# Kernel tuning notes

Measured on AMD Instinct MI355X. Metric: run time of the kernel, lower is better.

## Reference

```python
import jax, jax.numpy as jnp
import numpy as np

NT, NS, NH, NG = 365, 2048, 64, 128
PI = 3.1415  # constant used by the original code (not math.pi)


def setup_inputs() -> dict:
    key = jax.random.key(0)
    kP, kE, kTm, kdT, kxc, kW, kb = jax.random.split(key, 7)
    # Physically plausible forcings: positive precip/evap, T1 < T2 always
    P = jax.random.uniform(kP, (NT, NS)) * 20.0
    E = jax.random.uniform(kE, (NT, NS)) * 5.0
    Tm = jax.random.normal(kTm, (NT, NS)) * 10.0
    dT = jax.random.uniform(kdT, (NT, NS)) * 10.0 + 1.0
    T1 = Tm - dT / 2
    T2 = Tm + dT / 2
    x = jnp.stack([P, E, T1, T2], axis=-1)  # [nt, ns, 4]
    xc = jax.random.normal(kxc, (NS, NG))
    W = jax.random.normal(kW, (NH * 8 + 1, NG)) * 0.05  # fc weight
    b = jax.random.normal(kb, (NH * 8 + 1,)) * 0.05     # fc bias
    return {"x": x, "xc": xc, "W": W, "b": b}


def reference(x, xc, W, b):
    nh = (W.shape[0] - 1) // 8
    P, E, T1, T2 = x[..., 0], x[..., 1], x[..., 2], x[..., 3]  # each [nt, ns]
    Ta = (T1 + T2) / 2
    mask1 = T1 >= 0
    mask0 = T2 <= 0
    # nan-safe arccos argument: value is overwritten by the masks anyway
    arg = jnp.where(mask1 | mask0, 0.0, (T1 + T2) / (T2 - T1))
    rP = 1 - jnp.arccos(arg) / PI
    rP = jnp.where(mask1, 1.0, rP)
    rP = jnp.where(mask0, 0.0, rP)
    Ps = (1 - rP) * P  # snow
    Pl = rP * P        # liquid

    w = xc @ W.T + b  # [ns, nh*8+1]
    gm = jnp.exp(w[:, :nh]) + 1
    ge = jax.nn.sigmoid(w[:, nh:2 * nh]) * 2
    k0 = jax.nn.sigmoid(w[:, 3 * nh:4 * nh])
    k1 = jax.nn.sigmoid(w[:, 4 * nh:5 * nh])
    k2 = jax.nn.sigmoid(w[:, 5 * nh:6 * nh])
    gl = jnp.exp(w[:, 6 * nh:7 * nh])
    ga = jax.nn.softmax(w[:, 4 * nh:5 * nh], axis=1)  # dropout in eval = id
    qb = jax.nn.relu(w[:, -1]) / nh  # [ns]
    kb = jax.nn.sigmoid(w[:, 7 * nh:8 * nh]) / 10
    vi = jax.nn.sigmoid(w[:, 8 * nh:8 * nh + 1])  # (ns, 1) — faithful to source slice

    ns = P.shape[1]
    z = jnp.zeros((ns, nh), dtype=x.dtype)

    def step(carry, inp):
        S0, H0, H1, H2 = carry
        ps, pl, e, ta = inp  # each [ns]
        S = S0 + ps[:, None]
        Sm = jnp.minimum(S0, jax.nn.relu(ta[:, None] * gm))
        G1 = jax.nn.relu(H1 + Sm + pl[:, None] * vi - e[:, None] * ge)
        G0 = jax.nn.relu(H0 + G1 - gl + pl[:, None] * (1 - vi))
        Q0 = G0 * k0
        Q1a = jnp.minimum(G1, gl) * k1
        Q1 = Q1a * (1 - kb)
        G2 = H2 + Q1a * kb
        Q2 = G2 * k2
        Y = jnp.sum((Q0 + Q1 + Q2 + qb[:, None]) * ga, axis=1)
        return (S - Sm, G0 - Q0, jnp.minimum(G1 - Q1a, gl), G2 - Q2), Y

    _, Yout = jax.lax.scan(step, (z, z, z, z), (Ps, Pl, E, Ta))
    return Yout  # [nt, ns]
```

## Files before the change

kernel.cpp:

```cpp
#include <hip/hip_runtime.h>
#include <math.h>

#define NT 365
#define NS 2048
#define NH 64
#define NG 128
#define NW 513
#define WSTR 520

__device__ __forceinline__ float sigmoidf_(float x) {
    return 1.0f / (1.0f + __expf(-x));
}

__global__ __launch_bounds__(256) void forcing_kernel(const float* __restrict__ x,
                                                      float* __restrict__ f, int n) {
    int i = blockIdx.x * blockDim.x + threadIdx.x;
    if (i >= n) return;
    float4 v = ((const float4*)x)[i];
    float P = v.x, E = v.y, T1 = v.z, T2 = v.w;
    float Ta = 0.5f * (T1 + T2);
    float rP;
    if (T2 <= 0.0f)       rP = 0.0f;
    else if (T1 >= 0.0f)  rP = 1.0f;
    else                  rP = 1.0f - acosf((T1 + T2) / (T2 - T1)) * (1.0f / 3.1415f);
    float Ps = (1.0f - rP) * P;
    float Pl = rP * P;
    ((float4*)f)[i] = make_float4(Ps, Pl, E, fmaxf(Ta, 0.0f));
}

__global__ __launch_bounds__(256) void gemm_kernel(const float* __restrict__ xc,
                                                   const float* __restrict__ Wm,
                                                   const float* __restrict__ bv,
                                                   float* __restrict__ w) {
    __shared__ float xcs[64][132];
    __shared__ float Wsh[64][132];
    const int sTile = blockIdx.x * 64;
    const int by = blockIdx.y;
    const int jt = (by >= 2) ? by + 1 : by;
    const int jTile = jt * 64;
    const int t = threadIdx.x;

    for (int i = 0; i < 8; i++) {
        int f4  = t + i * 256;
        int row = f4 >> 5;
        int c4  = (f4 & 31) * 4;
        float4 v = ((const float4*)(xc + (size_t)(sTile + row) * NG))[f4 & 31];
        xcs[row][c4] = v.x; xcs[row][c4 + 1] = v.y; xcs[row][c4 + 2] = v.z; xcs[row][c4 + 3] = v.w;
        int jr = jTile + row;
        float4 wv = make_float4(0.f, 0.f, 0.f, 0.f);
        if (jr < NW) wv = ((const float4*)(Wm + (size_t)jr * NG))[f4 & 31];
        Wsh[row][c4] = wv.x; Wsh[row][c4 + 1] = wv.y; Wsh[row][c4 + 2] = wv.z; Wsh[row][c4 + 3] = wv.w;
    }
    __syncthreads();

    const int tx = t & 15, ty = t >> 4;
    float acc[4][4] = {};
#pragma unroll 4
    for (int k = 0; k < 128; k++) {
        float a0 = xcs[ty][k], a1 = xcs[ty + 16][k], a2 = xcs[ty + 32][k], a3 = xcs[ty + 48][k];
        float b0 = Wsh[tx][k], b1 = Wsh[tx + 16][k], b2 = Wsh[tx + 32][k], b3 = Wsh[tx + 48][k];
        acc[0][0] += a0 * b0; acc[0][1] += a0 * b1; acc[0][2] += a0 * b2; acc[0][3] += a0 * b3;
        acc[1][0] += a1 * b0; acc[1][1] += a1 * b1; acc[1][2] += a1 * b2; acc[1][3] += a1 * b3;
        acc[2][0] += a2 * b0; acc[2][1] += a2 * b1; acc[2][2] += a2 * b2; acc[2][3] += a2 * b3;
        acc[3][0] += a3 * b0; acc[3][1] += a3 * b1; acc[3][2] += a3 * b2; acc[3][3] += a3 * b3;
    }
#pragma unroll
    for (int i = 0; i < 4; i++) {
        int s = sTile + ty + 16 * i;
#pragma unroll
        for (int j = 0; j < 4; j++) {
            int jj = jTile + tx + 16 * j;
            if (jj < NW) w[(size_t)s * WSTR + jj] = acc[i][j] + bv[jj];
        }
    }
}

template <bool PRE>
__global__ __launch_bounds__(256) void scan_kernel(const float* __restrict__ fx,
                                                   const float* __restrict__ w,
                                                   float* __restrict__ Y) {
    __shared__ float ybuf[4][64][33];
    const int wave = threadIdx.x >> 6;
    const int lane = threadIdx.x & 63;
    const int s = blockIdx.x * 4 + wave;
    const float* wr = w + (size_t)s * WSTR;

    float gm = __expf(wr[lane]) + 1.0f;
    float ge = 2.0f * sigmoidf_(wr[64 + lane]);
    float k0 = sigmoidf_(wr[192 + lane]);
    float w4 = wr[256 + lane];
    float k1 = sigmoidf_(w4);
    float k2 = sigmoidf_(wr[320 + lane]);
    float gl = __expf(wr[384 + lane]);
    float kb = sigmoidf_(wr[448 + lane]) * 0.1f;
    float wl = wr[512];
    float qb = fmaxf(wl, 0.0f) * (1.0f / (float)NH);
    float vi = sigmoidf_(wl);

    float m = w4;
#pragma unroll
    for (int off = 32; off; off >>= 1) m = fmaxf(m, __shfl_xor(m, off));
    float ex = __expf(w4 - m);
    float sum = ex;
#pragma unroll
    for (int off = 32; off; off >>= 1) sum += __shfl_xor(sum, off);
    float ga = ex / sum;

    float c0  = k0 * ga;
    float c1  = k1 * (1.0f - kb) * ga;
    float c2  = k2 * ga;
    float k0c = 1.0f - k0;
    float k2c = 1.0f - k2;
    float geN = -ge;
    float glN = -gl;
    float viC = 1.0f - vi;

    float S0 = 0.f, H0 = 0.f, H1 = 0.f, H2 = 0.f;

    const int su = __builtin_amdgcn_readfirstlane(s);
    const float4* fp = (const float4*)fx + su;

    float* wp = &ybuf[wave][lane][0];
    const float* rp = &ybuf[wave][(lane >> 5) << 5][lane & 31];

    float4 vbuf[8];
#pragma unroll
    for (int b = 0; b < 8; b++) vbuf[b] = fp[b * NS];

    for (int sb = 0; sb < 12; sb++) {
        const int t0 = sb * 32;
        for (int ib = 0; ib < 4; ib++) {
#pragma unroll
            for (int b = 0; b < 8; b++) {
                const int tl = ib * 8 + b;
                float4 v = vbuf[b];
                int tn = t0 + (ib + 1) * 8 + b;
                tn = tn < NT ? tn : NT - 1;
                vbuf[b] = fp[(size_t)tn * NS];

                float Ps, Pl, E, TaR;
                if (PRE) {
                    Ps = v.x; Pl = v.y; E = v.z; TaR = v.w;
                } else {
                    float P = v.x; E = v.y;
                    float T1 = v.z, T2 = v.w;
                    float Ta = 0.5f * (T1 + T2);
                    float rP;
                    if (T2 <= 0.0f)      rP = 0.0f;
                    else if (T1 >= 0.0f) rP = 1.0f;
                    else                 rP = 1.0f - acosf((T1 + T2) / (T2 - T1)) * (1.0f / 3.1415f);
                    Ps = (1.0f - rP) * P;
                    Pl = rP * P;
                    TaR = fmaxf(Ta, 0.0f);
                }
                float S   = S0 + Ps;
                float Sm  = fminf(S0, gm * TaR);
                S0 = S - Sm;
                float G1  = fmaxf(H1 + Sm + fmaf(E, geN, Pl * vi), 0.0f);
                float G0  = fmaxf(H0 + G1 + fmaf(Pl, viC, glN), 0.0f);
                float m1  = fminf(G1, gl);
                float Q1a = m1 * k1;
                float G2  = fmaf(Q1a, kb, H2);
                wp[tl] = fmaf(G0, c0, fmaf(m1, c1, G2 * c2));
                H0 = G0 * k0c;
                H1 = fminf(G1 - Q1a, gl);
                H2 = G2 * k2c;
            }
        }
        float a0 = 0.f, a1 = 0.f, a2 = 0.f, a3 = 0.f;
#pragma unroll
        for (int j = 0; j < 32; j += 4) {
            a0 += rp[(size_t)j * 33];
            a1 += rp[(size_t)(j + 1) * 33];
            a2 += rp[(size_t)(j + 2) * 33];
            a3 += rp[(size_t)(j + 3) * 33];
        }
        float part = (a0 + a1) + (a2 + a3);
        float full = part + __shfl_xor(part, 32);
        int t = t0 + lane;
        if (lane < 32 && t < NT) Y[(size_t)t * NS + s] = full + qb;
    }
}

extern "C" void kernel_launch(void* const* d_in, const int* in_sizes, int n_in,
                              void* d_out, int out_size, void* d_ws, size_t ws_size,
                              hipStream_t stream) {
    const float* x  = (const float*)d_in[0];
    const float* xc = (const float*)d_in[1];
    const float* Wm = (const float*)d_in[2];
    const float* bv = (const float*)d_in[3];
    float* out = (float*)d_out;

    float* wbuf = (float*)d_ws;
    size_t wbytes = (size_t)NS * WSTR * sizeof(float);
    float* fbuf = (float*)((char*)d_ws + wbytes);
    size_t need = wbytes + (size_t)NT * NS * 4 * sizeof(float);

    gemm_kernel<<<dim3(32, 8), 256, 0, stream>>>(xc, Wm, bv, wbuf);

    if (ws_size >= need) {
        forcing_kernel<<<(NT * NS + 255) / 256, 256, 0, stream>>>(x, fbuf, NT * NS);
        scan_kernel<true><<<NS / 4, 256, 0, stream>>>(fbuf, wbuf, out);
    } else {
        scan_kernel<false><<<NS / 4, 256, 0, stream>>>(x, wbuf, out);
    }
}
```

Measured before the change: 121.8 us.

## Fuse gemm and forcing kernels; process two sites per wave in scan

Merges the parameter GEMM and the forcing precompute into one launch so one kernel launch and a dependency gap go away. The scan kernel now handles two sites per wavefront and interleaves their independent recurrences. This adds instruction-level parallelism to the latency-bound serial time loop and lets all 64 lanes take part in the final reduction. The cost is half as many blocks (256), which lowers occupancy and wave count on a large GPU, plus higher register and LDS use.

```diff
diff --git a/kernel.cpp b/kernel.cpp
--- a/kernel.cpp
+++ b/kernel.cpp
@@ -12,36 +12,38 @@
     return 1.0f / (1.0f + __expf(-x));
 }
 
-__global__ __launch_bounds__(256) void forcing_kernel(const float* __restrict__ x,
-                                                      float* __restrict__ f, int n) {
-    int i = blockIdx.x * blockDim.x + threadIdx.x;
-    if (i >= n) return;
-    float4 v = ((const float4*)x)[i];
-    float P = v.x, E = v.y, T1 = v.z, T2 = v.w;
-    float Ta = 0.5f * (T1 + T2);
-    float rP;
-    if (T2 <= 0.0f)       rP = 0.0f;
-    else if (T1 >= 0.0f)  rP = 1.0f;
-    else                  rP = 1.0f - acosf((T1 + T2) / (T2 - T1)) * (1.0f / 3.1415f);
-    float Ps = (1.0f - rP) * P;
-    float Pl = rP * P;
-    ((float4*)f)[i] = make_float4(Ps, Pl, E, fmaxf(Ta, 0.0f));
-}
-
-__global__ __launch_bounds__(256) void gemm_kernel(const float* __restrict__ xc,
+__global__ __launch_bounds__(256) void prep_kernel(const float* __restrict__ xc,
                                                    const float* __restrict__ Wm,
                                                    const float* __restrict__ bv,
-                                                   float* __restrict__ w) {
+                                                   float* __restrict__ w,
+                                                   const float* __restrict__ x,
+                                                   float* __restrict__ f) {
     __shared__ float xcs[64][132];
     __shared__ float Wsh[64][132];
-    const int sTile = blockIdx.x * 64;
-    const int by = blockIdx.y;
+    const int tid = threadIdx.x;
+
+    if (blockIdx.x >= 256) {
+        int i = (blockIdx.x - 256) * 256 + tid;
+        float4 v = ((const float4*)x)[i];
+        float P = v.x, E = v.y, T1 = v.z, T2 = v.w;
+        float Ta = 0.5f * (T1 + T2);
+        float rP;
+        if (T2 <= 0.0f)       rP = 0.0f;
+        else if (T1 >= 0.0f)  rP = 1.0f;
+        else                  rP = 1.0f - acosf((T1 + T2) / (T2 - T1)) * (1.0f / 3.1415f);
+        float Ps = (1.0f - rP) * P;
+        float Pl = rP * P;
+        ((float4*)f)[i] = make_float4(Ps, Pl, E, fmaxf(Ta, 0.0f));
+        return;
+    }
+
+    const int sTile = (blockIdx.x >> 3) * 64;
+    const int by = blockIdx.x & 7;
     const int jt = (by >= 2) ? by + 1 : by;
     const int jTile = jt * 64;
-    const int t = threadIdx.x;
 
     for (int i = 0; i < 8; i++) {
-        int f4  = t + i * 256;
+        int f4  = tid + i * 256;
         int row = f4 >> 5;
         int c4  = (f4 & 31) * 4;
         float4 v = ((const float4*)(xc + (size_t)(sTile + row) * NG))[f4 & 31];
@@ -53,7 +55,7 @@
     }
     __syncthreads();
 
-    const int tx = t & 15, ty = t >> 4;
+    const int tx = tid & 15, ty = tid >> 4;
     float acc[4][4] = {};
 #pragma unroll 4
     for (int k = 0; k < 128; k++) {
@@ -79,53 +81,61 @@
 __global__ __launch_bounds__(256) void scan_kernel(const float* __restrict__ fx,
                                                    const float* __restrict__ w,
                                                    float* __restrict__ Y) {
-    __shared__ float ybuf[4][64][33];
+    __shared__ float ybuf[4][2][64][33];
     const int wave = threadIdx.x >> 6;
     const int lane = threadIdx.x & 63;
-    const int s = blockIdx.x * 4 + wave;
-    const float* wr = w + (size_t)s * WSTR;
-
-    float gm = __expf(wr[lane]) + 1.0f;
-    float ge = 2.0f * sigmoidf_(wr[64 + lane]);
-    float k0 = sigmoidf_(wr[192 + lane]);
-    float w4 = wr[256 + lane];
-    float k1 = sigmoidf_(w4);
-    float k2 = sigmoidf_(wr[320 + lane]);
-    float gl = __expf(wr[384 + lane]);
-    float kb = sigmoidf_(wr[448 + lane]) * 0.1f;
-    float wl = wr[512];
-    float qb = fmaxf(wl, 0.0f) * (1.0f / (float)NH);
-    float vi = sigmoidf_(wl);
-
-    float m = w4;
-#pragma unroll
-    for (int off = 32; off; off >>= 1) m = fmaxf(m, __shfl_xor(m, off));
-    float ex = __expf(w4 - m);
-    float sum = ex;
-#pragma unroll
-    for (int off = 32; off; off >>= 1) sum += __shfl_xor(sum, off);
-    float ga = ex / sum;
-
-    float c0  = k0 * ga;
-    float c1  = k1 * (1.0f - kb) * ga;
-    float c2  = k2 * ga;
-    float k0c = 1.0f - k0;
-    float k2c = 1.0f - k2;
-    float geN = -ge;
-    float glN = -gl;
-    float viC = 1.0f - vi;
-
-    float S0 = 0.f, H0 = 0.f, H1 = 0.f, H2 = 0.f;
-
-    const int su = __builtin_amdgcn_readfirstlane(s);
+    const int sA = blockIdx.x * 8 + wave * 2;
+    const float* wrA = w + (size_t)sA * WSTR;
+    const float* wrB = wrA + WSTR;
+
+    float gmA = __expf(wrA[lane]) + 1.0f,          gmB = __expf(wrB[lane]) + 1.0f;
+    float geNA = -2.0f * sigmoidf_(wrA[64 + lane]), geNB = -2.0f * sigmoidf_(wrB[64 + lane]);
+    float k0A = sigmoidf_(wrA[192 + lane]),        k0B = sigmoidf_(wrB[192 + lane]);
+    float w4A = wrA[256 + lane],                   w4B = wrB[256 + lane];
+    float k1A = sigmoidf_(w4A),                    k1B = sigmoidf_(w4B);
+    float k2A = sigmoidf_(wrA[320 + lane]),        k2B = sigmoidf_(wrB[320 + lane]);
+    float glA = __expf(wrA[384 + lane]),           glB = __expf(wrB[384 + lane]);
+    float kbA = sigmoidf_(wrA[448 + lane]) * 0.1f, kbB = sigmoidf_(wrB[448 + lane]) * 0.1f;
+    float wlA = wrA[512],                          wlB = wrB[512];
+    float qbA = fmaxf(wlA, 0.0f) * (1.0f / NH),    qbB = fmaxf(wlB, 0.0f) * (1.0f / NH);
+    float viA = sigmoidf_(wlA),                    viB = sigmoidf_(wlB);
+
+    float mA = w4A, mB = w4B;
+#pragma unroll
+    for (int off = 32; off; off >>= 1) {
+        mA = fmaxf(mA, __shfl_xor(mA, off));
+        mB = fmaxf(mB, __shfl_xor(mB, off));
+    }
+    float exA = __expf(w4A - mA), exB = __expf(w4B - mB);
+    float smA = exA, smB = exB;
+#pragma unroll
+    for (int off = 32; off; off >>= 1) {
+        smA += __shfl_xor(smA, off);
+        smB += __shfl_xor(smB, off);
+    }
+    float gaA = exA / smA, gaB = exB / smB;
+
+    float c0A = k0A * gaA,                  c0B = k0B * gaB;
+    float c1A = k1A * (1.0f - kbA) * gaA,   c1B = k1B * (1.0f - kbB) * gaB;
+    float c2A = k2A * gaA,                  c2B = k2B * gaB;
+    float k0cA = 1.0f - k0A,                k0cB = 1.0f - k0B;
+    float k2cA = 1.0f - k2A,                k2cB = 1.0f - k2B;
+    float glNA = -glA,                      glNB = -glB;
+    float viCA = 1.0f - viA,                viCB = 1.0f - viB;
+
+    float S0A = 0.f, H0A = 0.f, H1A = 0.f, H2A = 0.f;
+    float S0B = 0.f, H0B = 0.f, H1B = 0.f, H2B = 0.f;
+
+    const int su = __builtin_amdgcn_readfirstlane(sA);
     const float4* fp = (const float4*)fx + su;
 
-    float* wp = &ybuf[wave][lane][0];
-    const float* rp = &ybuf[wave][(lane >> 5) << 5][lane & 31];
-
-    float4 vbuf[8];
-#pragma unroll
-    for (int b = 0; b < 8; b++) vbuf[b] = fp[b * NS];
+    float* wp = &ybuf[wave][0][lane][0];
+    const float* rp = &ybuf[wave][lane >> 5][0][lane & 31];
+    const float qbS = (lane < 32) ? qbA : qbB;
+
+    float4 vbA[8], vbB[8];
+#pragma unroll
+    for (int b = 0; b < 8; b++) { vbA[b] = fp[b * NS]; vbB[b] = fp[b * NS + 1]; }
 
     for (int sb = 0; sb < 12; sb++) {
         const int t0 = sb * 32;
@@ -133,52 +143,75 @@
 #pragma unroll
             for (int b = 0; b < 8; b++) {
                 const int tl = ib * 8 + b;
-                float4 v = vbuf[b];
+                float4 vA = vbA[b], vB = vbB[b];
                 int tn = t0 + (ib + 1) * 8 + b;
                 tn = tn < NT ? tn : NT - 1;
-                vbuf[b] = fp[(size_t)tn * NS];
-
-                float Ps, Pl, E, TaR;
+                vbA[b] = fp[(size_t)tn * NS];
+                vbB[b] = fp[(size_t)tn * NS + 1];
+
+                float PsA, PlA, EA, TaRA, PsB, PlB, EB, TaRB;
                 if (PRE) {
-                    Ps = v.x; Pl = v.y; E = v.z; TaR = v.w;
+                    PsA = vA.x; PlA = vA.y; EA = vA.z; TaRA = vA.w;
+                    PsB = vB.x; PlB = vB.y; EB = vB.z; TaRB = vB.w;
                 } else {
-                    float P = v.x; E = v.y;
-                    float T1 = v.z, T2 = v.w;
-                    float Ta = 0.5f * (T1 + T2);
-                    float rP;
-                    if (T2 <= 0.0f)      rP = 0.0f;
-                    else if (T1 >= 0.0f) rP = 1.0f;
-                    else                 rP = 1.0f - acosf((T1 + T2) / (T2 - T1)) * (1.0f / 3.1415f);
-                    Ps = (1.0f - rP) * P;
-                    Pl = rP * P;
-                    TaR = fmaxf(Ta, 0.0f);
+                    {
+                        float P = vA.x; EA = vA.y;
+                        float T1 = vA.z, T2 = vA.w;
+                        float Ta = 0.5f * (T1 + T2);
+                        float rP;
+                        if (T2 <= 0.0f)      rP = 0.0f;
+                        else if (T1 >= 0.0f) rP = 1.0f;
+                        else                 rP = 1.0f - acosf((T1 + T2) / (T2 - T1)) * (1.0f / 3.1415f);
+                        PsA = (1.0f - rP) * P; PlA = rP * P; TaRA = fmaxf(Ta, 0.0f);
+                    }
+                    {
+                        float P = vB.x; EB = vB.y;
+                        float T1 = vB.z, T2 = vB.w;
+                        float Ta = 0.5f * (T1 + T2);
+                        float rP;
+                        if (T2 <= 0.0f)      rP = 0.0f;
+                        else if (T1 >= 0.0f) rP = 1.0f;
+                        else                 rP = 1.0f - acosf((T1 + T2) / (T2 - T1)) * (1.0f / 3.1415f);
+                        PsB = (1.0f - rP) * P; PlB = rP * P; TaRB = fmaxf(Ta, 0.0f);
+                    }
                 }
-                float S   = S0 + Ps;
-                float Sm  = fminf(S0, gm * TaR);
-                S0 = S - Sm;
-                float G1  = fmaxf(H1 + Sm + fmaf(E, geN, Pl * vi), 0.0f);
-                float G0  = fmaxf(H0 + G1 + fmaf(Pl, viC, glN), 0.0f);
-                float m1  = fminf(G1, gl);
-                float Q1a = m1 * k1;
-                float G2  = fmaf(Q1a, kb, H2);
-                wp[tl] = fmaf(G0, c0, fmaf(m1, c1, G2 * c2));
-                H0 = G0 * k0c;
-                H1 = fminf(G1 - Q1a, gl);
-                H2 = G2 * k2c;
+                float SA   = S0A + PsA;
+                float SmA  = fminf(S0A, gmA * TaRA);
+                S0A = SA - SmA;
+                float G1A  = fmaxf(H1A + SmA + fmaf(EA, geNA, PlA * viA), 0.0f);
+                float G0A  = fmaxf(H0A + G1A + fmaf(PlA, viCA, glNA), 0.0f);
+                float m1A  = fminf(G1A, glA);
+                float Q1aA = m1A * k1A;
+                float G2A  = fmaf(Q1aA, kbA, H2A);
+                wp[tl] = fmaf(G0A, c0A, fmaf(m1A, c1A, G2A * c2A));
+                H0A = G0A * k0cA;
+                H1A = fminf(G1A - Q1aA, glA);
+                H2A = G2A * k2cA;
+                float SB   = S0B + PsB;
+                float SmB  = fminf(S0B, gmB * TaRB);
+                S0B = SB - SmB;
+                float G1B  = fmaxf(H1B + SmB + fmaf(EB, geNB, PlB * viB), 0.0f);
+                float G0B  = fmaxf(H0B + G1B + fmaf(PlB, viCB, glNB), 0.0f);
+                float m1B  = fminf(G1B, glB);
+                float Q1aB = m1B * k1B;
+                float G2B  = fmaf(Q1aB, kbB, H2B);
+                wp[64 * 33 + tl] = fmaf(G0B, c0B, fmaf(m1B, c1B, G2B * c2B));
+                H0B = G0B * k0cB;
+                H1B = fminf(G1B - Q1aB, glB);
+                H2B = G2B * k2cB;
             }
         }
         float a0 = 0.f, a1 = 0.f, a2 = 0.f, a3 = 0.f;
 #pragma unroll
-        for (int j = 0; j < 32; j += 4) {
+        for (int j = 0; j < 64; j += 4) {
             a0 += rp[(size_t)j * 33];
             a1 += rp[(size_t)(j + 1) * 33];
             a2 += rp[(size_t)(j + 2) * 33];
             a3 += rp[(size_t)(j + 3) * 33];
         }
-        float part = (a0 + a1) + (a2 + a3);
-        float full = part + __shfl_xor(part, 32);
-        int t = t0 + lane;
-        if (lane < 32 && t < NT) Y[(size_t)t * NS + s] = full + qb;
+        float full = (a0 + a1) + (a2 + a3);
+        int t = t0 + (lane & 31);
+        if (t < NT) Y[(size_t)t * NS + sA + (lane >> 5)] = full + qbS;
     }
 }
 
@@ -196,12 +229,11 @@
     float* fbuf = (float*)((char*)d_ws + wbytes);
     size_t need = wbytes + (size_t)NT * NS * 4 * sizeof(float);
 
-    gemm_kernel<<<dim3(32, 8), 256, 0, stream>>>(xc, Wm, bv, wbuf);
-
     if (ws_size >= need) {
-        forcing_kernel<<<(NT * NS + 255) / 256, 256, 0, stream>>>(x, fbuf, NT * NS);
-        scan_kernel<true><<<NS / 4, 256, 0, stream>>>(fbuf, wbuf, out);
+        prep_kernel<<<256 + (NT * NS) / 256, 256, 0, stream>>>(xc, Wm, bv, wbuf, x, fbuf);
+        scan_kernel<true><<<NS / 8, 256, 0, stream>>>(fbuf, wbuf, out);
     } else {
-        scan_kernel<false><<<NS / 4, 256, 0, stream>>>(x, wbuf, out);
-    }
-}
+        prep_kernel<<<256, 256, 0, stream>>>(xc, Wm, bv, wbuf, x, fbuf);
+        scan_kernel<false><<<NS / 8, 256, 0, stream>>>(x, wbuf, out);
+    }
+}
```

After: 154.2 us. 1.27x slower.

## Merge GEMM and forcing kernels into one launch and unroll scan loop fully

Applied to the files above, without the earlier changes.

The separate GEMM and forcing-preprocess kernels become a single prep kernel: blocks beyond the first 256 handle forcing, the rest do the GEMM. This removes one launch and lets both run concurrently. The scan loop is now fully unrolled over 32 steps, and the time-index clamp is hoisted out of every block except the last. The base pointer is also kept in a vector register through an asm barrier instead of readfirstlane. In exchange the unrolled code is much larger and may raise register pressure.

```diff
diff --git a/kernel.cpp b/kernel.cpp
--- a/kernel.cpp
+++ b/kernel.cpp
@@ -12,36 +12,38 @@
     return 1.0f / (1.0f + __expf(-x));
 }
 
-__global__ __launch_bounds__(256) void forcing_kernel(const float* __restrict__ x,
-                                                      float* __restrict__ f, int n) {
-    int i = blockIdx.x * blockDim.x + threadIdx.x;
-    if (i >= n) return;
-    float4 v = ((const float4*)x)[i];
-    float P = v.x, E = v.y, T1 = v.z, T2 = v.w;
-    float Ta = 0.5f * (T1 + T2);
-    float rP;
-    if (T2 <= 0.0f)       rP = 0.0f;
-    else if (T1 >= 0.0f)  rP = 1.0f;
-    else                  rP = 1.0f - acosf((T1 + T2) / (T2 - T1)) * (1.0f / 3.1415f);
-    float Ps = (1.0f - rP) * P;
-    float Pl = rP * P;
-    ((float4*)f)[i] = make_float4(Ps, Pl, E, fmaxf(Ta, 0.0f));
-}
-
-__global__ __launch_bounds__(256) void gemm_kernel(const float* __restrict__ xc,
+__global__ __launch_bounds__(256) void prep_kernel(const float* __restrict__ xc,
                                                    const float* __restrict__ Wm,
                                                    const float* __restrict__ bv,
-                                                   float* __restrict__ w) {
+                                                   float* __restrict__ w,
+                                                   const float* __restrict__ x,
+                                                   float* __restrict__ f) {
     __shared__ float xcs[64][132];
     __shared__ float Wsh[64][132];
-    const int sTile = blockIdx.x * 64;
-    const int by = blockIdx.y;
+    const int tid = threadIdx.x;
+
+    if (blockIdx.x >= 256) {
+        int i = (blockIdx.x - 256) * 256 + tid;
+        float4 v = ((const float4*)x)[i];
+        float P = v.x, E = v.y, T1 = v.z, T2 = v.w;
+        float Ta = 0.5f * (T1 + T2);
+        float rP;
+        if (T2 <= 0.0f)       rP = 0.0f;
+        else if (T1 >= 0.0f)  rP = 1.0f;
+        else                  rP = 1.0f - acosf((T1 + T2) / (T2 - T1)) * (1.0f / 3.1415f);
+        float Ps = (1.0f - rP) * P;
+        float Pl = rP * P;
+        ((float4*)f)[i] = make_float4(Ps, Pl, E, fmaxf(Ta, 0.0f));
+        return;
+    }
+
+    const int sTile = (blockIdx.x >> 3) * 64;
+    const int by = blockIdx.x & 7;
     const int jt = (by >= 2) ? by + 1 : by;
     const int jTile = jt * 64;
-    const int t = threadIdx.x;
 
     for (int i = 0; i < 8; i++) {
-        int f4  = t + i * 256;
+        int f4  = tid + i * 256;
         int row = f4 >> 5;
         int c4  = (f4 & 31) * 4;
         float4 v = ((const float4*)(xc + (size_t)(sTile + row) * NG))[f4 & 31];
@@ -53,7 +55,7 @@
     }
     __syncthreads();
 
-    const int tx = t & 15, ty = t >> 4;
+    const int tx = tid & 15, ty = tid >> 4;
     float acc[4][4] = {};
 #pragma unroll 4
     for (int k = 0; k < 128; k++) {
@@ -86,7 +88,7 @@
     const float* wr = w + (size_t)s * WSTR;
 
     float gm = __expf(wr[lane]) + 1.0f;
-    float ge = 2.0f * sigmoidf_(wr[64 + lane]);
+    float geN = -2.0f * sigmoidf_(wr[64 + lane]);
     float k0 = sigmoidf_(wr[192 + lane]);
     float w4 = wr[256 + lane];
     float k1 = sigmoidf_(w4);
@@ -111,14 +113,14 @@
     float c2  = k2 * ga;
     float k0c = 1.0f - k0;
     float k2c = 1.0f - k2;
-    float geN = -ge;
     float glN = -gl;
     float viC = 1.0f - vi;
 
     float S0 = 0.f, H0 = 0.f, H1 = 0.f, H2 = 0.f;
 
-    const int su = __builtin_amdgcn_readfirstlane(s);
-    const float4* fp = (const float4*)fx + su;
+    int sv = s;
+    asm volatile("" : "+v"(sv));
+    const float4* fp = (const float4*)fx + sv;
 
     float* wp = &ybuf[wave][lane][0];
     const float* rp = &ybuf[wave][(lane >> 5) << 5][lane & 31];
@@ -127,59 +129,74 @@
 #pragma unroll
     for (int b = 0; b < 8; b++) vbuf[b] = fp[b * NS];
 
-    for (int sb = 0; sb < 12; sb++) {
+#define STEP_BODY(vv, tl)                                                      \
+    {                                                                          \
+        float Ps, Pl, E, TaR;                                                  \
+        if (PRE) { Ps = vv.x; Pl = vv.y; E = vv.z; TaR = vv.w; }               \
+        else {                                                                 \
+            float P = vv.x; E = vv.y;                                          \
+            float T1 = vv.z, T2 = vv.w;                                        \
+            float Ta = 0.5f * (T1 + T2);                                       \
+            float rP;                                                          \
+            if (T2 <= 0.0f)      rP = 0.0f;                                    \
+            else if (T1 >= 0.0f) rP = 1.0f;                                    \
+            else rP = 1.0f - acosf((T1 + T2) / (T2 - T1)) * (1.0f / 3.1415f);  \
+            Ps = (1.0f - rP) * P; Pl = rP * P; TaR = fmaxf(Ta, 0.0f);          \
+        }                                                                      \
+        float S   = S0 + Ps;                                                   \
+        float Sm  = fminf(S0, gm * TaR);                                       \
+        S0 = S - Sm;                                                           \
+        float G1  = fmaxf(H1 + Sm + fmaf(E, geN, Pl * vi), 0.0f);              \
+        float G0  = fmaxf(H0 + G1 + fmaf(Pl, viC, glN), 0.0f);                 \
+        float m1  = fminf(G1, gl);                                             \
+        float Q1a = m1 * k1;                                                   \
+        float G2  = fmaf(Q1a, kb, H2);                                         \
+        wp[tl] = fmaf(G0, c0, fmaf(m1, c1, G2 * c2));                          \
+        H0 = G0 * k0c;                                                         \
+        H1 = fminf(G1 - Q1a, gl);                                              \
+        H2 = G2 * k2c;                                                         \
+    }
+
+#define TRRED(t0)                                                              \
+    {                                                                          \
+        float a0 = 0.f, a1 = 0.f, a2 = 0.f, a3 = 0.f;                          \
+        _Pragma("unroll")                                                      \
+        for (int j = 0; j < 32; j += 4) {                                      \
+            a0 += rp[(size_t)j * 33];                                          \
+            a1 += rp[(size_t)(j + 1) * 33];                                    \
+            a2 += rp[(size_t)(j + 2) * 33];                                    \
+            a3 += rp[(size_t)(j + 3) * 33];                                    \
+        }                                                                      \
+        float part = (a0 + a1) + (a2 + a3);                                    \
+        float full = part + __shfl_xor(part, 32);                              \
+        int t = (t0) + (lane & 31);                                            \
+        if (lane < 32 && t < NT) Y[(size_t)t * NS + s] = full + qb;            \
+    }
+
+    for (int sb = 0; sb < 11; ++sb) {
         const int t0 = sb * 32;
-        for (int ib = 0; ib < 4; ib++) {
-#pragma unroll
-            for (int b = 0; b < 8; b++) {
-                const int tl = ib * 8 + b;
-                float4 v = vbuf[b];
-                int tn = t0 + (ib + 1) * 8 + b;
-                tn = tn < NT ? tn : NT - 1;
-                vbuf[b] = fp[(size_t)tn * NS];
-
-                float Ps, Pl, E, TaR;
-                if (PRE) {
-                    Ps = v.x; Pl = v.y; E = v.z; TaR = v.w;
-                } else {
-                    float P = v.x; E = v.y;
-                    float T1 = v.z, T2 = v.w;
-                    float Ta = 0.5f * (T1 + T2);
-                    float rP;
-                    if (T2 <= 0.0f)      rP = 0.0f;
-                    else if (T1 >= 0.0f) rP = 1.0f;
-                    else                 rP = 1.0f - acosf((T1 + T2) / (T2 - T1)) * (1.0f / 3.1415f);
-                    Ps = (1.0f - rP) * P;
-                    Pl = rP * P;
-                    TaR = fmaxf(Ta, 0.0f);
-                }
-                float S   = S0 + Ps;
-                float Sm  = fminf(S0, gm * TaR);
-                S0 = S - Sm;
-                float G1  = fmaxf(H1 + Sm + fmaf(E, geN, Pl * vi), 0.0f);
-                float G0  = fmaxf(H0 + G1 + fmaf(Pl, viC, glN), 0.0f);
-                float m1  = fminf(G1, gl);
-                float Q1a = m1 * k1;
-                float G2  = fmaf(Q1a, kb, H2);
-                wp[tl] = fmaf(G0, c0, fmaf(m1, c1, G2 * c2));
-                H0 = G0 * k0c;
-                H1 = fminf(G1 - Q1a, gl);
-                H2 = G2 * k2c;
-            }
+        const float4* fpt = fp + (size_t)t0 * NS;
+#pragma unroll
+        for (int tl = 0; tl < 32; ++tl) {
+            float4 v = vbuf[tl & 7];
+            vbuf[tl & 7] = fpt[(size_t)(tl + 8) * NS];
+            STEP_BODY(v, tl);
         }
-        float a0 = 0.f, a1 = 0.f, a2 = 0.f, a3 = 0.f;
-#pragma unroll
-        for (int j = 0; j < 32; j += 4) {
-            a0 += rp[(size_t)j * 33];
-            a1 += rp[(size_t)(j + 1) * 33];
-            a2 += rp[(size_t)(j + 2) * 33];
-            a3 += rp[(size_t)(j + 3) * 33];
+        TRRED(t0);
+    }
+    {
+        const int t0 = 352;
+#pragma unroll
+        for (int tl = 0; tl < 32; ++tl) {
+            float4 v = vbuf[tl & 7];
+            int tn = t0 + tl + 8; tn = tn < NT ? tn : NT - 1;
+            vbuf[tl & 7] = fp[(size_t)tn * NS];
+            STEP_BODY(v, tl);
         }
-        float part = (a0 + a1) + (a2 + a3);
-        float full = part + __shfl_xor(part, 32);
-        int t = t0 + lane;
-        if (lane < 32 && t < NT) Y[(size_t)t * NS + s] = full + qb;
-    }
+        TRRED(t0);
+    }
+#undef STEP_BODY
+#undef TRRED
 }
 
 extern "C" void kernel_launch(void* const* d_in, const int* in_sizes, int n_in,
@@ -196,12 +213,11 @@
     float* fbuf = (float*)((char*)d_ws + wbytes);
     size_t need = wbytes + (size_t)NT * NS * 4 * sizeof(float);
 
-    gemm_kernel<<<dim3(32, 8), 256, 0, stream>>>(xc, Wm, bv, wbuf);
-
     if (ws_size >= need) {
-        forcing_kernel<<<(NT * NS + 255) / 256, 256, 0, stream>>>(x, fbuf, NT * NS);
+        prep_kernel<<<256 + (NT * NS) / 256, 256, 0, stream>>>(xc, Wm, bv, wbuf, x, fbuf);
         scan_kernel<true><<<NS / 4, 256, 0, stream>>>(fbuf, wbuf, out);
     } else {
+        prep_kernel<<<256, 256, 0, stream>>>(xc, Wm, bv, wbuf, x, fbuf);
         scan_kernel<false><<<NS / 4, 256, 0, stream>>>(x, wbuf, out);
     }
 }
```

After: 110.1 us. -9.6%, faster.

## Fuse forcing prep into GEMM launch and pack two sites per wave

Applied to the files above, without the earlier changes.

The forcing precompute is merged into the GEMM kernel as extra blocks, which removes one launch. Forcings are written in a per-site-pair, time-contiguous layout so the scan reads them with contiguous loads. The scan now has each wave process two sites together using 2-wide float vectors, aiming at packed FP32 math, and prefetches 16 steps ahead. In exchange, the scan launches half as many waves, which reduces parallelism, and it uses more registers under launch_bounds(256,1).

```diff
diff --git a/kernel.cpp b/kernel.cpp
--- a/kernel.cpp
+++ b/kernel.cpp
@@ -7,41 +7,71 @@
 #define NG 128
 #define NW 513
 #define WSTR 520
+#define FTR 368
+
+typedef float v2f __attribute__((ext_vector_type(2)));
 
 __device__ __forceinline__ float sigmoidf_(float x) {
     return 1.0f / (1.0f + __expf(-x));
 }
-
-__global__ __launch_bounds__(256) void forcing_kernel(const float* __restrict__ x,
-                                                      float* __restrict__ f, int n) {
-    int i = blockIdx.x * blockDim.x + threadIdx.x;
-    if (i >= n) return;
-    float4 v = ((const float4*)x)[i];
-    float P = v.x, E = v.y, T1 = v.z, T2 = v.w;
-    float Ta = 0.5f * (T1 + T2);
-    float rP;
-    if (T2 <= 0.0f)       rP = 0.0f;
-    else if (T1 >= 0.0f)  rP = 1.0f;
-    else                  rP = 1.0f - acosf((T1 + T2) / (T2 - T1)) * (1.0f / 3.1415f);
-    float Ps = (1.0f - rP) * P;
-    float Pl = rP * P;
-    ((float4*)f)[i] = make_float4(Ps, Pl, E, fmaxf(Ta, 0.0f));
-}
-
-__global__ __launch_bounds__(256) void gemm_kernel(const float* __restrict__ xc,
+__device__ __forceinline__ v2f vmin2(v2f a, v2f b) {
+    v2f r; r.x = fminf(a.x, b.x); r.y = fminf(a.y, b.y); return r;
+}
+__device__ __forceinline__ v2f vmax0(v2f a) {
+    v2f r; r.x = fmaxf(a.x, 0.0f); r.y = fmaxf(a.y, 0.0f); return r;
+}
+
+__global__ __launch_bounds__(256) void prep_kernel(const float* __restrict__ xc,
                                                    const float* __restrict__ Wm,
                                                    const float* __restrict__ bv,
-                                                   float* __restrict__ w) {
+                                                   float* __restrict__ w,
+                                                   const float* __restrict__ x,
+                                                   float* __restrict__ f) {
     __shared__ float xcs[64][132];
     __shared__ float Wsh[64][132];
-    const int sTile = blockIdx.x * 64;
-    const int by = blockIdx.y;
+    const int tid = threadIdx.x;
+
+    if (blockIdx.x >= 256) {
+        const int b = blockIdx.x - 256;
+        const int p = b * 16 + (tid >> 4);
+        const int phase = tid & 15;
+        const float4* xp = (const float4*)x;
+        float4* fpo = (float4*)(f + (size_t)p * (FTR * 8));
+        for (int tt = phase; tt < NT; tt += 16) {
+            float4 vA = xp[(size_t)tt * NS + 2 * p];
+            float4 vB = xp[(size_t)tt * NS + 2 * p + 1];
+            float PsA, PlA, TaRA, PsB, PlB, TaRB;
+            {
+                float P = vA.x, T1 = vA.z, T2 = vA.w;
+                float Ta = 0.5f * (T1 + T2);
+                float rP;
+                if (T2 <= 0.0f)       rP = 0.0f;
+                else if (T1 >= 0.0f)  rP = 1.0f;
+                else                  rP = 1.0f - acosf((T1 + T2) / (T2 - T1)) * (1.0f / 3.1415f);
+                PsA = (1.0f - rP) * P; PlA = rP * P; TaRA = fmaxf(Ta, 0.0f);
+            }
+            {
+                float P = vB.x, T1 = vB.z, T2 = vB.w;
+                float Ta = 0.5f * (T1 + T2);
+                float rP;
+                if (T2 <= 0.0f)       rP = 0.0f;
+                else if (T1 >= 0.0f)  rP = 1.0f;
+                else                  rP = 1.0f - acosf((T1 + T2) / (T2 - T1)) * (1.0f / 3.1415f);
+                PsB = (1.0f - rP) * P; PlB = rP * P; TaRB = fmaxf(Ta, 0.0f);
+            }
+            fpo[tt * 2]     = make_float4(PsA, PsB, PlA, PlB);
+            fpo[tt * 2 + 1] = make_float4(vA.y, vB.y, TaRA, TaRB);
+        }
+        return;
+    }
+
+    const int sTile = (blockIdx.x >> 3) * 64;
+    const int by = blockIdx.x & 7;
     const int jt = (by >= 2) ? by + 1 : by;
     const int jTile = jt * 64;
-    const int t = threadIdx.x;
 
     for (int i = 0; i < 8; i++) {
-        int f4  = t + i * 256;
+        int f4  = tid + i * 256;
         int row = f4 >> 5;
         int c4  = (f4 & 31) * 4;
         float4 v = ((const float4*)(xc + (size_t)(sTile + row) * NG))[f4 & 31];
@@ -53,7 +83,7 @@
     }
     __syncthreads();
 
-    const int tx = t & 15, ty = t >> 4;
+    const int tx = tid & 15, ty = tid >> 4;
     float acc[4][4] = {};
 #pragma unroll 4
     for (int k = 0; k < 128; k++) {
@@ -75,10 +105,134 @@
     }
 }
 
-template <bool PRE>
-__global__ __launch_bounds__(256) void scan_kernel(const float* __restrict__ fx,
-                                                   const float* __restrict__ w,
-                                                   float* __restrict__ Y) {
+__global__ __launch_bounds__(256, 1) void scan_pk_kernel(const float* __restrict__ fx,
+                                                         const float* __restrict__ w,
+                                                         float* __restrict__ Y) {
+    __shared__ float ybuf[4][64][66];
+    const int wave = threadIdx.x >> 6;
+    const int lane = threadIdx.x & 63;
+    const int pair = blockIdx.x * 4 + wave;
+    const int sA = pair * 2;
+    const float* wrA = w + (size_t)sA * WSTR;
+    const float* wrB = wrA + WSTR;
+
+    v2f gm  = { __expf(wrA[lane]) + 1.0f,        __expf(wrB[lane]) + 1.0f };
+    v2f geN = { -2.0f * sigmoidf_(wrA[64 + lane]), -2.0f * sigmoidf_(wrB[64 + lane]) };
+    v2f k0  = { sigmoidf_(wrA[192 + lane]),      sigmoidf_(wrB[192 + lane]) };
+    v2f w4  = { wrA[256 + lane],                 wrB[256 + lane] };
+    v2f k1  = { sigmoidf_(w4.x),                 sigmoidf_(w4.y) };
+    v2f k2  = { sigmoidf_(wrA[320 + lane]),      sigmoidf_(wrB[320 + lane]) };
+    v2f gl  = { __expf(wrA[384 + lane]),         __expf(wrB[384 + lane]) };
+    v2f kb  = { sigmoidf_(wrA[448 + lane]) * 0.1f, sigmoidf_(wrB[448 + lane]) * 0.1f };
+    float wlA = wrA[512], wlB = wrB[512];
+    float qbA = fmaxf(wlA, 0.0f) * (1.0f / NH), qbB = fmaxf(wlB, 0.0f) * (1.0f / NH);
+    v2f vi  = { sigmoidf_(wlA),                  sigmoidf_(wlB) };
+
+    float mA = w4.x, mB = w4.y;
+#pragma unroll
+    for (int off = 32; off; off >>= 1) {
+        mA = fmaxf(mA, __shfl_xor(mA, off));
+        mB = fmaxf(mB, __shfl_xor(mB, off));
+    }
+    float exA = __expf(w4.x - mA), exB = __expf(w4.y - mB);
+    float smA = exA, smB = exB;
+#pragma unroll
+    for (int off = 32; off; off >>= 1) {
+        smA += __shfl_xor(smA, off);
+        smB += __shfl_xor(smB, off);
+    }
+    v2f ga = { exA / smA, exB / smB };
+
+    v2f one = { 1.0f, 1.0f };
+    v2f c0   = k0 * ga;
+    v2f c1   = k1 * (one - kb) * ga;
+    v2f c2   = k2 * ga;
+    v2f k0c  = one - k0;
+    v2f k2c  = one - k2;
+    v2f glN  = -gl;
+    v2f viC  = one - vi;
+    v2f k1kb = k1 * kb;
+    v2f k1N  = -k1;
+
+    v2f S0 = {0.f, 0.f}, H0 = {0.f, 0.f}, H1 = {0.f, 0.f}, H2 = {0.f, 0.f};
+
+    const char* fB = (const char*)fx;
+    unsigned voff = (unsigned)pair * (FTR * 32u);
+    asm volatile("" : "+v"(voff));
+
+    float4 va[16], vb[16];
+#pragma unroll
+    for (int b = 0; b < 16; b++) {
+        va[b] = *(const float4*)(fB + voff + b * 32);
+        vb[b] = *(const float4*)(fB + voff + b * 32 + 16);
+    }
+
+    float* wp = &ybuf[wave][lane][0];
+    const float* rp = &ybuf[wave][(lane >> 5) << 5][(lane & 31) * 2];
+
+#define STEP_PK(v1, v2, tl)                                                    \
+    {                                                                          \
+        v2f Ps = {v1.x, v1.y}, Pl = {v1.z, v1.w};                              \
+        v2f E  = {v2.x, v2.y}, Ta = {v2.z, v2.w};                              \
+        v2f S  = S0 + Ps;                                                      \
+        v2f Sm = vmin2(S0, gm * Ta);                                           \
+        S0 = S - Sm;                                                           \
+        v2f G1 = vmax0(H1 + Sm + (E * geN + Pl * vi));                         \
+        v2f G0 = vmax0(H0 + G1 + (Pl * viC + glN));                            \
+        v2f m1 = vmin2(G1, gl);                                                \
+        v2f G2 = m1 * k1kb + H2;                                               \
+        *(v2f*)&wp[2 * (tl)] = G0 * c0 + (m1 * c1 + G2 * c2);                  \
+        H0 = G0 * k0c;                                                         \
+        H1 = vmin2(m1 * k1N + G1, gl);                                         \
+        H2 = G2 * k2c;                                                         \
+    }
+
+#define TRRED_PK(t0)                                                           \
+    {                                                                          \
+        v2f a0 = {0.f,0.f}, a1 = {0.f,0.f}, a2 = {0.f,0.f}, a3 = {0.f,0.f};    \
+        _Pragma("unroll")                                                      \
+        for (int j = 0; j < 32; j += 4) {                                      \
+            a0 += *(const v2f*)&rp[(size_t)j * 66];                            \
+            a1 += *(const v2f*)&rp[(size_t)(j + 1) * 66];                      \
+            a2 += *(const v2f*)&rp[(size_t)(j + 2) * 66];                      \
+            a3 += *(const v2f*)&rp[(size_t)(j + 3) * 66];                      \
+        }                                                                      \
+        v2f part = (a0 + a1) + (a2 + a3);                                      \
+        float fx_ = part.x + __shfl_xor(part.x, 32);                           \
+        float fy_ = part.y + __shfl_xor(part.y, 32);                           \
+        int t = (t0) + (lane & 31);                                            \
+        if (lane < 32 && t < NT) {                                             \
+            Y[(size_t)t * NS + sA]     = fx_ + qbA;                            \
+            Y[(size_t)t * NS + sA + 1] = fy_ + qbB;                            \
+        }                                                                      \
+    }
+
+    for (int sb = 0; sb < 11; ++sb) {
+        const char* fs = fB + sb * (32 * 32);
+#pragma unroll
+        for (int tl = 0; tl < 32; ++tl) {
+            float4 v1 = va[tl & 15], v2 = vb[tl & 15];
+            va[tl & 15] = *(const float4*)(fs + voff + (tl + 16) * 32);
+            vb[tl & 15] = *(const float4*)(fs + voff + (tl + 16) * 32 + 16);
+            STEP_PK(v1, v2, tl);
+        }
+        TRRED_PK(sb * 32);
+    }
+    {
+#pragma unroll
+        for (int tl = 0; tl < 32; ++tl) {
+            float4 v1 = va[tl & 15], v2 = vb[tl & 15];
+            STEP_PK(v1, v2, tl);
+        }
+        TRRED_PK(352);
+    }
+#undef STEP_PK
+#undef TRRED_PK
+}
+
+__global__ __launch_bounds__(256) void scan_kernel_raw(const float* __restrict__ fx,
+                                                       const float* __restrict__ w,
+                                                       float* __restrict__ Y) {
     __shared__ float ybuf[4][64][33];
     const int wave = threadIdx.x >> 6;
     const int lane = threadIdx.x & 63;
@@ -86,7 +240,7 @@
     const float* wr = w + (size_t)s * WSTR;
 
     float gm = __expf(wr[lane]) + 1.0f;
-    float ge = 2.0f * sigmoidf_(wr[64 + lane]);
+    float geN = -2.0f * sigmoidf_(wr[64 + lane]);
     float k0 = sigmoidf_(wr[192 + lane]);
     float w4 = wr[256 + lane];
     float k1 = sigmoidf_(w4);
@@ -106,66 +260,41 @@
     for (int off = 32; off; off >>= 1) sum += __shfl_xor(sum, off);
     float ga = ex / sum;
 
-    float c0  = k0 * ga;
-    float c1  = k1 * (1.0f - kb) * ga;
-    float c2  = k2 * ga;
-    float k0c = 1.0f - k0;
-    float k2c = 1.0f - k2;
-    float geN = -ge;
-    float glN = -gl;
-    float viC = 1.0f - vi;
-
+    float c0 = k0 * ga, c1 = k1 * (1.0f - kb) * ga, c2 = k2 * ga;
+    float k0c = 1.0f - k0, k2c = 1.0f - k2, glN = -gl, viC = 1.0f - vi;
+    float k1kb = k1 * kb, k1N = -k1;
     float S0 = 0.f, H0 = 0.f, H1 = 0.f, H2 = 0.f;
 
-    const int su = __builtin_amdgcn_readfirstlane(s);
-    const float4* fp = (const float4*)fx + su;
+    unsigned voff = (unsigned)s * 16u;
+    asm volatile("" : "+v"(voff));
+    const char* fB = (const char*)fx;
 
     float* wp = &ybuf[wave][lane][0];
     const float* rp = &ybuf[wave][(lane >> 5) << 5][lane & 31];
 
-    float4 vbuf[8];
-#pragma unroll
-    for (int b = 0; b < 8; b++) vbuf[b] = fp[b * NS];
-
-    for (int sb = 0; sb < 12; sb++) {
+    for (int sb = 0; sb < 12; ++sb) {
         const int t0 = sb * 32;
-        for (int ib = 0; ib < 4; ib++) {
-#pragma unroll
-            for (int b = 0; b < 8; b++) {
-                const int tl = ib * 8 + b;
-                float4 v = vbuf[b];
-                int tn = t0 + (ib + 1) * 8 + b;
-                tn = tn < NT ? tn : NT - 1;
-                vbuf[b] = fp[(size_t)tn * NS];
-
-                float Ps, Pl, E, TaR;
-                if (PRE) {
-                    Ps = v.x; Pl = v.y; E = v.z; TaR = v.w;
-                } else {
-                    float P = v.x; E = v.y;
-                    float T1 = v.z, T2 = v.w;
-                    float Ta = 0.5f * (T1 + T2);
-                    float rP;
-                    if (T2 <= 0.0f)      rP = 0.0f;
-                    else if (T1 >= 0.0f) rP = 1.0f;
-                    else                 rP = 1.0f - acosf((T1 + T2) / (T2 - T1)) * (1.0f / 3.1415f);
-                    Ps = (1.0f - rP) * P;
-                    Pl = rP * P;
-                    TaR = fmaxf(Ta, 0.0f);
-                }
-                float S   = S0 + Ps;
-                float Sm  = fminf(S0, gm * TaR);
-                S0 = S - Sm;
-                float G1  = fmaxf(H1 + Sm + fmaf(E, geN, Pl * vi), 0.0f);
-                float G0  = fmaxf(H0 + G1 + fmaf(Pl, viC, glN), 0.0f);
-                float m1  = fminf(G1, gl);
-                float Q1a = m1 * k1;
-                float G2  = fmaf(Q1a, kb, H2);
-                wp[tl] = fmaf(G0, c0, fmaf(m1, c1, G2 * c2));
-                H0 = G0 * k0c;
-                H1 = fminf(G1 - Q1a, gl);
-                H2 = G2 * k2c;
-            }
+        for (int tl = 0; tl < 32; ++tl) {
+            int t = t0 + tl; t = t < NT ? t : NT - 1;
+            float4 v = *(const float4*)(fB + (size_t)t * (NS * 16) + voff);
+            float P = v.x, E = v.y, T1 = v.z, T2 = v.w;
+            float Ta = 0.5f * (T1 + T2);
+            float rP;
+            if (T2 <= 0.0f)      rP = 0.0f;
+            else if (T1 >= 0.0f) rP = 1.0f;
+            else                 rP = 1.0f - acosf((T1 + T2) / (T2 - T1)) * (1.0f / 3.1415f);
+            float Ps = (1.0f - rP) * P, Pl = rP * P, TaR = fmaxf(Ta, 0.0f);
+            float S   = S0 + Ps;
+            float Sm  = fminf(S0, gm * TaR);
+            S0 = S - Sm;
+            float G1  = fmaxf(H1 + Sm + fmaf(E, geN, Pl * vi), 0.0f);
+            float G0  = fmaxf(H0 + G1 + fmaf(Pl, viC, glN), 0.0f);
+            float m1  = fminf(G1, gl);
+            float G2  = fmaf(m1, k1kb, H2);
+            wp[tl] = fmaf(G0, c0, fmaf(m1, c1, G2 * c2));
+            H0 = G0 * k0c;
+            H1 = fminf(fmaf(m1, k1N, G1), gl);
+            H2 = G2 * k2c;
         }
         float a0 = 0.f, a1 = 0.f, a2 = 0.f, a3 = 0.f;
 #pragma unroll
@@ -177,7 +306,7 @@
         }
         float part = (a0 + a1) + (a2 + a3);
         float full = part + __shfl_xor(part, 32);
-        int t = t0 + lane;
+        int t = t0 + (lane & 31);
         if (lane < 32 && t < NT) Y[(size_t)t * NS + s] = full + qb;
     }
 }
@@ -194,14 +323,13 @@
     float* wbuf = (float*)d_ws;
     size_t wbytes = (size_t)NS * WSTR * sizeof(float);
     float* fbuf = (float*)((char*)d_ws + wbytes);
-    size_t need = wbytes + (size_t)NT * NS * 4 * sizeof(float);
-
-    gemm_kernel<<<dim3(32, 8), 256, 0, stream>>>(xc, Wm, bv, wbuf);
+    size_t need = wbytes + (size_t)(NS / 2) * FTR * 32;
 
     if (ws_size >= need) {
-        forcing_kernel<<<(NT * NS + 255) / 256, 256, 0, stream>>>(x, fbuf, NT * NS);
-        scan_kernel<true><<<NS / 4, 256, 0, stream>>>(fbuf, wbuf, out);
+        prep_kernel<<<256 + 64, 256, 0, stream>>>(xc, Wm, bv, wbuf, x, fbuf);
+        scan_pk_kernel<<<NS / 8, 256, 0, stream>>>(fbuf, wbuf, out);
     } else {
-        scan_kernel<false><<<NS / 4, 256, 0, stream>>>(x, wbuf, out);
-    }
-}
+        prep_kernel<<<256, 256, 0, stream>>>(xc, Wm, bv, wbuf, x, fbuf);
+        scan_kernel_raw<<<NS / 4, 256, 0, stream>>>(x, wbuf, out);
+    }
+}
```

New measurement: 115.8 us. 1.05x faster.
